# Optimization experiments

Hardware: AMD Instinct MI355X
Metric: run time of the kernel (lower is better)

The kernel has to match this reference:

```python
import jax, jax.numpy as jnp
import numpy as np
import math

B, S, D, H = 2, 2048, 512, 8
HD = D // H

def setup_inputs() -> dict:
    key = jax.random.key(0)
    ks = jax.random.split(key, 13)
    scale = 1.0 / math.sqrt(D)
    inp = {
        "q_in": jax.random.normal(ks[0], (B, S, D), jnp.float32),
        "k_in": jax.random.normal(ks[1], (B, S, D), jnp.float32),
        "v_in": jax.random.normal(ks[2], (B, S, D), jnp.float32),
        "mask": jax.random.randint(ks[3], (B, 1, S, S), 0, 2, jnp.int32),
        "W1": jax.random.uniform(ks[4], (D, D), jnp.float32, -scale, scale),
        "b1": jax.random.uniform(ks[5], (D,), jnp.float32, -scale, scale),
        "W2": jax.random.uniform(ks[6], (D, D), jnp.float32, -scale, scale),
        "b2": jax.random.uniform(ks[7], (D,), jnp.float32, -scale, scale),
        "W3": jax.random.uniform(ks[8], (D, D), jnp.float32, -scale, scale),
        "b3": jax.random.uniform(ks[9], (D,), jnp.float32, -scale, scale),
        "Wo": jax.random.uniform(ks[10], (D, D), jnp.float32, -scale, scale),
        "bo": jax.random.uniform(ks[11], (D,), jnp.float32, -scale, scale),
    }
    return inp

def reference(q_in, k_in, v_in, mask, W1, b1, W2, b2, W3, b3, Wo, bo):
    # Linear projections (torch Linear: y = x @ W.T + b)
    q = q_in @ W1.T + b1  # [B,S,D]
    k = k_in @ W2.T + b2
    v = v_in @ W3.T + b3
    # split heads -> [B,H,S,HD]
    def split(x):
        return x.reshape(B, S, H, HD).transpose(0, 2, 1, 3)
    q, k, v = split(q), split(k), split(v)
    scores = jnp.einsum("bhqd,bhkd->bhqk", q, k) / math.sqrt(HD)
    scores = jnp.where(mask == 0, jnp.float32(-1e9), scores)
    attn = jax.nn.softmax(scores, axis=-1)
    out = jnp.einsum("bhqk,bhkd->bhqd", attn, v)  # [B,H,S,HD]
    out = out.transpose(0, 2, 1, 3).reshape(B, S, D)
    return out @ Wo.T + bo
```

## Files before the change

### kernel.cpp

```cpp
#include <hip/hip_runtime.h>
#include <hip/hip_bf16.h>
#include <math.h>

constexpr int B_ = 2, S_ = 2048, D_ = 512, H_ = 8, HD_ = 64;
constexpr int M_ = B_ * S_;
constexpr int NT_ = S_ / 64;
constexpr int NSPLIT = 2;
constexpr int NT2 = NT_ / NSPLIT;
constexpr int ROWS = B_ * S_ * H_;

typedef short s16x8 __attribute__((ext_vector_type(8)));
typedef float f32x4 __attribute__((ext_vector_type(4)));
typedef unsigned short u16;
typedef unsigned long long u64;

#define SWZ(b) ((b) ^ ((((b) >> 7) & 7) << 4))

constexpr float SCL = 0.18033688f;

static __device__ __forceinline__ unsigned int cvt_pk2(float lo, float hi) {
  __hip_bfloat162 h = __float22bfloat162_rn(make_float2(lo, hi));
  return *(unsigned int*)&h;
}
static __device__ __forceinline__ u16 cvt1(float f) {
  __hip_bfloat16 h = __float2bfloat16(f);
  return *(u16*)&h;
}
static __device__ __forceinline__ uint4 pack8(float4 a, float4 b) {
  uint4 r;
  r.x = cvt_pk2(a.x, a.y); r.y = cvt_pk2(a.z, a.w);
  r.z = cvt_pk2(b.x, b.y); r.w = cvt_pk2(b.z, b.w);
  return r;
}

#define QKV_STEP(BUF, T)                                                      \
  {                                                                           \
    const bool more_ = ((T) < 7);                                             \
    if (more_) {                                                              \
      const int o4 = ((T) + 1) * 16;                                          \
      fx[0] = Xb[o4];  fx[1] = Xb[o4 + 1];  fx[2] = Xb[o4 + 2];  fx[3] = Xb[o4 + 3]; \
      fw0[0] = W0b[o4]; fw0[1] = W0b[o4 + 1]; fw0[2] = W0b[o4 + 2]; fw0[3] = W0b[o4 + 3]; \
      fw1[0] = W1b[o4]; fw1[1] = W1b[o4 + 1]; fw1[2] = W1b[o4 + 2]; fw1[3] = W1b[o4 + 3]; \
    }                                                                         \
    __builtin_amdgcn_s_setprio(1);                                            \
    _Pragma("unroll")                                                         \
    for (int kw = 0; kw < 2; ++kw) {                                          \
      s16x8 af0 = *(const s16x8*)(shb + SWZ((BUF)*24576 + (wm*32 + l15)*128 + kw*64 + lg*16)); \
      s16x8 af1 = *(const s16x8*)(shb + SWZ((BUF)*24576 + (wm*32 + 16 + l15)*128 + kw*64 + lg*16)); \
      s16x8 b00 = *(const s16x8*)(shb + SWZ((BUF)*24576 + 8192 + (wn*32 + l15)*128 + kw*64 + lg*16)); \
      s16x8 b01 = *(const s16x8*)(shb + SWZ((BUF)*24576 + 8192 + (wn*32 + 16 + l15)*128 + kw*64 + lg*16)); \
      s16x8 b10 = *(const s16x8*)(shb + SWZ((BUF)*24576 + 16384 + (wn*32 + l15)*128 + kw*64 + lg*16)); \
      s16x8 b11 = *(const s16x8*)(shb + SWZ((BUF)*24576 + 16384 + (wn*32 + 16 + l15)*128 + kw*64 + lg*16)); \
      acc[0][0][0] = __builtin_amdgcn_mfma_f32_16x16x32_bf16(af0, b00, acc[0][0][0], 0, 0, 0); \
      acc[0][0][1] = __builtin_amdgcn_mfma_f32_16x16x32_bf16(af0, b01, acc[0][0][1], 0, 0, 0); \
      acc[0][1][0] = __builtin_amdgcn_mfma_f32_16x16x32_bf16(af1, b00, acc[0][1][0], 0, 0, 0); \
      acc[0][1][1] = __builtin_amdgcn_mfma_f32_16x16x32_bf16(af1, b01, acc[0][1][1], 0, 0, 0); \
      acc[1][0][0] = __builtin_amdgcn_mfma_f32_16x16x32_bf16(af0, b10, acc[1][0][0], 0, 0, 0); \
      acc[1][0][1] = __builtin_amdgcn_mfma_f32_16x16x32_bf16(af0, b11, acc[1][0][1], 0, 0, 0); \
      acc[1][1][0] = __builtin_amdgcn_mfma_f32_16x16x32_bf16(af1, b10, acc[1][1][0], 0, 0, 0); \
      acc[1][1][1] = __builtin_amdgcn_mfma_f32_16x16x32_bf16(af1, b11, acc[1][1][1], 0, 0, 0); \
    }                                                                         \
    __builtin_amdgcn_s_setprio(0);                                            \
    if (more_) {                                                              \
      char* p_ = shb + ((BUF) ^ 1) * 24576;                                   \
      *(uint4*)(p_ + SWZ(awb)) = pack8(fx[0], fx[1]);                         \
      *(uint4*)(p_ + SWZ(awb + 16)) = pack8(fx[2], fx[3]);                    \
      *(uint4*)(p_ + SWZ(b0wb)) = pack8(fw0[0], fw0[1]);                      \
      *(uint4*)(p_ + SWZ(b0wb + 16)) = pack8(fw0[2], fw0[3]);                 \
      *(uint4*)(p_ + SWZ(b1wb)) = pack8(fw1[0], fw1[1]);                      \
      *(uint4*)(p_ + SWZ(b1wb + 16)) = pack8(fw1[2], fw1[3]);                 \
    }                                                                         \
    __syncthreads();                                                          \
  }

__global__ __launch_bounds__(256) void gemm_qkv(
    const float* __restrict__ Xq, const float* __restrict__ Wq,
    const float* __restrict__ bq, u16* __restrict__ Yq,
    const float* __restrict__ Xk, const float* __restrict__ Wk,
    const float* __restrict__ bk, u16* __restrict__ Yk,
    const float* __restrict__ Xv, const float* __restrict__ Wv,
    const float* __restrict__ bv, u16* __restrict__ Yv,
    const int* __restrict__ mask, u64* __restrict__ mbits)
{
  const float* X; const float* W; const float* bias; u16* Y;
  const int z = blockIdx.z;
  if (z == 0)      { X = Xq; W = Wq; bias = bq; Y = Yq; }
  else if (z == 1) { X = Xk; W = Wk; bias = bk; Y = Yk; }
  else             { X = Xv; W = Wv; bias = bv; Y = Yv; }

  __shared__ __align__(128) char SH[2][24576];
  char* shb = &SH[0][0];

  const int tid = threadIdx.x;
  const int lane = tid & 63, w = tid >> 6;
  const int l15 = lane & 15, lg = lane >> 4;
  const int wm = w >> 1, wn = w & 1;
  const int m0 = blockIdx.x * 64, n0 = blockIdx.y * 128;
  const int sr = tid >> 2, sc = (tid & 3) * 16;

  const float4* Xb  = (const float4*)&X[(size_t)(m0 + sr) * D_ + sc];
  const float4* W0b = (const float4*)&W[(size_t)(n0 + sr) * D_ + sc];
  const float4* W1b = (const float4*)&W[(size_t)(n0 + 64 + sr) * D_ + sc];
  const int awb  = sr * 128 + (tid & 3) * 32;
  const int b0wb = 8192 + awb;
  const int b1wb = 16384 + awb;

  f32x4 acc[2][2][2];
#pragma unroll
  for (int nh = 0; nh < 2; ++nh)
#pragma unroll
    for (int i = 0; i < 2; ++i)
#pragma unroll
      for (int j = 0; j < 2; ++j) acc[nh][i][j] = (f32x4){0.f, 0.f, 0.f, 0.f};

  float4 fx[4], fw0[4], fw1[4];
#pragma unroll
  for (int i = 0; i < 4; ++i) { fx[i] = Xb[i]; fw0[i] = W0b[i]; fw1[i] = W1b[i]; }
  {
    char* p = shb;
    *(uint4*)(p + SWZ(awb)) = pack8(fx[0], fx[1]);
    *(uint4*)(p + SWZ(awb + 16)) = pack8(fx[2], fx[3]);
    *(uint4*)(p + SWZ(b0wb)) = pack8(fw0[0], fw0[1]);
    *(uint4*)(p + SWZ(b0wb + 16)) = pack8(fw0[2], fw0[3]);
    *(uint4*)(p + SWZ(b1wb)) = pack8(fw1[0], fw1[1]);
    *(uint4*)(p + SWZ(b1wb + 16)) = pack8(fw1[2], fw1[3]);
  }
  __syncthreads();

#pragma unroll 1
  for (int tt = 0; tt < 8; tt += 2) {
    QKV_STEP(0, tt)
    QKV_STEP(1, tt + 1)
  }

  const float oscale = (z == 0) ? SCL : 1.0f;

  if (z != 2) {
#pragma unroll
    for (int nh = 0; nh < 2; ++nh) {
      float bias_v[2];
      bias_v[0] = bias[n0 + nh * 64 + wn * 32 + l15];
      bias_v[1] = bias[n0 + nh * 64 + wn * 32 + 16 + l15];
#pragma unroll
      for (int am = 0; am < 2; ++am)
#pragma unroll
        for (int bn = 0; bn < 2; ++bn)
#pragma unroll
          for (int j = 0; j < 4; ++j) {
            const int row = m0 + wm * 32 + am * 16 + lg * 4 + j;
            const int col = n0 + nh * 64 + wn * 32 + bn * 16 + l15;
            Y[(size_t)row * D_ + col] = cvt1((acc[nh][am][bn][j] + bias_v[bn]) * oscale);
          }
    }
  } else {
    const int batch = m0 >> 11, sb = m0 & (S_ - 1);
#pragma unroll
    for (int nh = 0; nh < 2; ++nh) {
      const int hh = blockIdx.y * 2 + nh;
      float bias_v[2];
      bias_v[0] = bias[n0 + nh * 64 + wn * 32 + l15];
      bias_v[1] = bias[n0 + nh * 64 + wn * 32 + 16 + l15];
      __syncthreads();
#pragma unroll
      for (int am = 0; am < 2; ++am)
#pragma unroll
        for (int bn = 0; bn < 2; ++bn) {
          const int dd = wn * 32 + bn * 16 + l15;
          const int sl = wm * 32 + am * 16 + lg * 4;
          ushort4 pk;
          pk.x = cvt1(acc[nh][am][bn][0] + bias_v[bn]);
          pk.y = cvt1(acc[nh][am][bn][1] + bias_v[bn]);
          pk.z = cvt1(acc[nh][am][bn][2] + bias_v[bn]);
          pk.w = cvt1(acc[nh][am][bn][3] + bias_v[bn]);
          *(ushort4*)(shb + SWZ(dd * 128 + sl * 2)) = pk;
        }
      __syncthreads();
      const int cr = sr * 128 + (tid & 3) * 32;
      uint4 c0 = *(uint4*)(shb + SWZ(cr));
      uint4 c1 = *(uint4*)(shb + SWZ(cr + 16));
      u16* dst = &Y[(((size_t)batch * H_ + hh) * 64 + sr) * S_ + sb + sc];
      *(uint4*)dst = c0;
      *(uint4*)(dst + 8) = c1;
    }
  }

  {
    const int bid = blockIdx.x + blockIdx.y * gridDim.x +
                    blockIdx.z * gridDim.x * gridDim.y;
    const int gw = bid * 4 + w;
    const int ngroups = (B_ * S_ * NT_) / 4;
#pragma unroll 1
    for (int g = gw; g < ngroups; g += 3072) {
      const int4 v = *(const int4*)&mask[(size_t)g * 256 + lane * 4];
      u64 b0 = __ballot(v.x != 0);
      u64 b1 = __ballot(v.y != 0);
      u64 b2 = __ballot(v.z != 0);
      u64 b3 = __ballot(v.w != 0);
      if (lane < 4) {
        const int q = lane;
        u64 r = ((b0 >> (16 * q)) & 0xFFFFULL)
              | (((b1 >> (16 * q)) & 0xFFFFULL) << 16)
              | (((b2 >> (16 * q)) & 0xFFFFULL) << 32)
              | (((b3 >> (16 * q)) & 0xFFFFULL) << 48);
        mbits[(size_t)g * 4 + q] = r;
      }
    }
  }
}

#define OPROJ_STEP(BUF, T)                                                    \
  {                                                                           \
    const bool more_ = ((T) < 7);                                             \
    if (more_) {                                                              \
      const int k0 = ((T) + 1) * 64;                                          \
      ax[0] = ((const uint4*)(Xb + k0))[0];                                   \
      ax[1] = ((const uint4*)(Xb + k0))[1];                                   \
      const int o4 = ((T) + 1) * 16;                                          \
      fw[0] = Wb[o4]; fw[1] = Wb[o4 + 1]; fw[2] = Wb[o4 + 2]; fw[3] = Wb[o4 + 3]; \
    }                                                                         \
    __builtin_amdgcn_s_setprio(1);                                            \
    _Pragma("unroll")                                                         \
    for (int kw = 0; kw < 2; ++kw) {                                          \
      s16x8 af0 = *(const s16x8*)(shb + SWZ((BUF)*16384 + (wm*32 + l15)*128 + kw*64 + lg*16)); \
      s16x8 af1 = *(const s16x8*)(shb + SWZ((BUF)*16384 + (wm*32 + 16 + l15)*128 + kw*64 + lg*16)); \
      s16x8 bf0 = *(const s16x8*)(shb + SWZ((BUF)*16384 + 8192 + (wn*32 + l15)*128 + kw*64 + lg*16)); \
      s16x8 bf1 = *(const s16x8*)(shb + SWZ((BUF)*16384 + 8192 + (wn*32 + 16 + l15)*128 + kw*64 + lg*16)); \
      acc[0][0] = __builtin_amdgcn_mfma_f32_16x16x32_bf16(af0, bf0, acc[0][0], 0, 0, 0); \
      acc[0][1] = __builtin_amdgcn_mfma_f32_16x16x32_bf16(af0, bf1, acc[0][1], 0, 0, 0); \
      acc[1][0] = __builtin_amdgcn_mfma_f32_16x16x32_bf16(af1, bf0, acc[1][0], 0, 0, 0); \
      acc[1][1] = __builtin_amdgcn_mfma_f32_16x16x32_bf16(af1, bf1, acc[1][1], 0, 0, 0); \
    }                                                                         \
    __builtin_amdgcn_s_setprio(0);                                            \
    if (more_) {                                                              \
      char* p_ = shb + ((BUF) ^ 1) * 16384;                                   \
      *(uint4*)(p_ + SWZ(awb)) = ax[0];                                       \
      *(uint4*)(p_ + SWZ(awb + 16)) = ax[1];                                  \
      *(uint4*)(p_ + SWZ(bwb)) = pack8(fw[0], fw[1]);                         \
      *(uint4*)(p_ + SWZ(bwb + 16)) = pack8(fw[2], fw[3]);                    \
    }                                                                         \
    __syncthreads();                                                          \
  }

__global__ __launch_bounds__(256) void gemm_oproj(
    const u16* __restrict__ X, const float* __restrict__ W,
    const float* __restrict__ bias, float* __restrict__ Y)
{
  __shared__ __align__(128) u16 SH[2][2][64][64];
  char* shb = (char*)SH;

  const int tid = threadIdx.x;
  const int lane = tid & 63, w = tid >> 6;
  const int l15 = lane & 15, lg = lane >> 4;
  const int wm = w >> 1, wn = w & 1;
  const int m0 = blockIdx.x * 64, n0 = blockIdx.y * 64;
  const int sr = tid >> 2, sc = (tid & 3) * 16;

  const u16* Xb = X + (size_t)(m0 + sr) * D_ + sc;
  const float4* Wb = (const float4*)&W[(size_t)(n0 + sr) * D_ + sc];
  const int awb = sr * 128 + (tid & 3) * 32;
  const int bwb = 8192 + sr * 128 + (tid & 3) * 32;

  f32x4 acc[2][2];
#pragma unroll
  for (int i = 0; i < 2; ++i)
#pragma unroll
    for (int j = 0; j < 2; ++j) acc[i][j] = (f32x4){0.f, 0.f, 0.f, 0.f};

  uint4 ax[2]; float4 fw[4];
  ax[0] = ((const uint4*)Xb)[0]; ax[1] = ((const uint4*)Xb)[1];
#pragma unroll
  for (int i = 0; i < 4; ++i) fw[i] = Wb[i];
  {
    char* p = shb;
    *(uint4*)(p + SWZ(awb)) = ax[0];
    *(uint4*)(p + SWZ(awb + 16)) = ax[1];
    *(uint4*)(p + SWZ(bwb)) = pack8(fw[0], fw[1]);
    *(uint4*)(p + SWZ(bwb + 16)) = pack8(fw[2], fw[3]);
  }
  __syncthreads();

#pragma unroll 1
  for (int tt = 0; tt < 8; tt += 2) {
    OPROJ_STEP(0, tt)
    OPROJ_STEP(1, tt + 1)
  }

  float bias_v[2];
  bias_v[0] = bias[n0 + wn * 32 + l15];
  bias_v[1] = bias[n0 + wn * 32 + 16 + l15];
#pragma unroll
  for (int am = 0; am < 2; ++am)
#pragma unroll
    for (int bn = 0; bn < 2; ++bn)
#pragma unroll
      for (int j = 0; j < 4; ++j) {
        const int row = m0 + wm * 32 + am * 16 + lg * 4 + j;
        const int col = n0 + wn * 32 + bn * 16 + l15;
        Y[(size_t)row * D_ + col] = acc[am][bn][j] + bias_v[bn];
      }
}

__global__ __launch_bounds__(256) void attn_mfma(
    const u16* __restrict__ qp, const u16* __restrict__ kp,
    const u16* __restrict__ vt, const u64* __restrict__ mbits,
    float* __restrict__ po, float* __restrict__ pm, float* __restrict__ pl)
{
  const int fid = blockIdx.x + 32 * (blockIdx.y + 8 * blockIdx.z);
  const int d = (fid & 7) * 128 + (fid >> 3);
  const int bx = d & 31, by = (d >> 5) & 7, bz = d >> 8;

  const int b = bz >> 1, half = bz & 1;
  const int h = by;
  const int q0 = bx * 64;
  const int kt0 = half * (S_ / NSPLIT);
  const int tid = threadIdx.x;
  const int lane = tid & 63;
  const int w = tid >> 6;
  const int l15 = lane & 15, lg = lane >> 4;

  __shared__ __align__(128) u16 KV[2][2][64][64];
  __shared__ __align__(128) u16 Pl[4][16][64];
  char* kvb = (char*)KV;
  char* plb = (char*)Pl;

  const int qr = q0 + w * 16;

  const u16* qrow = qp + ((size_t)b * S_ + qr + l15) * D_ + h * HD_;
  const s16x8 qf0 = *(const s16x8*)(qrow + lg * 8);
  const s16x8 qf1 = *(const s16x8*)(qrow + 32 + lg * 8);

  s16x8 onesf;
#pragma unroll
  for (int i = 0; i < 8; ++i) onesf[i] = (short)0x3F80;

  f32x4 out[4];
#pragma unroll
  for (int dt = 0; dt < 4; ++dt) out[dt] = (f32x4){0.f, 0.f, 0.f, 0.f};
  float l_s = 0.f;

  const int sr = tid >> 2;
  const int sc = (tid & 3) * 16;
  const u16* kbase = kp + (size_t)b * S_ * D_ + h * HD_;
  const u16* vbase = vt + (((size_t)b * H_ + h) * 64 + sr) * (size_t)S_ + kt0 + sc;
  const u64* mrow = mbits + ((size_t)b * S_ + qr + l15) * NT_ + half * NT2;

  const int mX = (l15 & 7) << 4;
  const int rd_lo = ((l15 << 7) + lg * 16) ^ mX;
  const int rd_hi = rd_lo ^ 64;
  const int mW = (sr & 7) << 4;
  const int wr_lo = ((sr << 7) + (tid & 3) * 32) ^ mW;
  const int wr_hi = wr_lo ^ 16;
  const int pq = w * 2048 + l15 * 128;
  const int pw0 = (pq + lg * 8) ^ mX;
  const int pa_lo = (pq + lg * 16) ^ mX;
  const int pa_hi = pa_lo ^ 64;

  uint4 rk0, rk1, rv0, rv1;
  {
    const u16* ksrc = kbase + (size_t)(kt0 + sr) * D_ + sc;
    rk0 = *(const uint4*)ksrc; rk1 = *(const uint4*)(ksrc + 8);
    rv0 = *(const uint4*)vbase; rv1 = *(const uint4*)(vbase + 8);
    *(uint4*)(kvb + wr_lo) = rk0;
    *(uint4*)(kvb + wr_hi) = rk1;
    *(uint4*)(kvb + wr_lo + 8192) = rv0;
    *(uint4*)(kvb + wr_hi + 8192) = rv1;
  }
  u64 msk = mrow[0];
  __syncthreads();

#pragma unroll 1
  for (int t = 0; t < NT2; ++t) {
    const int cur = t & 1;
    const bool more = (t + 1 < NT2);
    u64 msk_n = 0;
    if (more) {
      const int kt = (t + 1) * 64;
      const u16* ksrc = kbase + (size_t)(kt0 + kt + sr) * D_ + sc;
      rk0 = *(const uint4*)ksrc; rk1 = *(const uint4*)(ksrc + 8);
      rv0 = *(const uint4*)(vbase + kt); rv1 = *(const uint4*)(vbase + kt + 8);
      msk_n = mrow[t + 1];
    }

    const unsigned mlo = (unsigned)(msk >> lg);
    const unsigned mhi = (unsigned)(msk >> (lg + 32));

    char* rb_lo = kvb + (cur << 14) + rd_lo;
    char* rb_hi = kvb + (cur << 14) + rd_hi;

    f32x4 z[4];
    __builtin_amdgcn_s_setprio(1);
#pragma unroll
    for (int t4 = 0; t4 < 4; ++t4) {
      s16x8 kb0 = *(const s16x8*)(rb_lo + t4 * 2048);
      s16x8 kb1 = *(const s16x8*)(rb_hi + t4 * 2048);
      f32x4 zz = (f32x4){0.f, 0.f, 0.f, 0.f};
      zz = __builtin_amdgcn_mfma_f32_16x16x32_bf16(kb0, qf0, zz, 0, 0, 0);
      zz = __builtin_amdgcn_mfma_f32_16x16x32_bf16(kb1, qf1, zz, 0, 0, 0);
      z[t4] = zz;
    }
    __builtin_amdgcn_s_setprio(0);

    float x[4][4];
#pragma unroll
    for (int t4 = 0; t4 < 4; ++t4) {
#pragma unroll
      for (int r = 0; r < 4; ++r) {
        const unsigned bit = (r < 2) ? ((mlo >> (16 * r + 4 * t4)) & 1u)
                                     : ((mhi >> (16 * (r - 2) + 4 * t4)) & 1u);
        float xv = bit ? z[t4][r] : -1.0e9f;
        x[t4][r] = exp2f(xv);
      }
    }

#pragma unroll
    for (int t4 = 0; t4 < 4; ++t4) {
      uint2 pk;
      pk.x = cvt_pk2(x[t4][0], x[t4][1]);
      pk.y = cvt_pk2(x[t4][2], x[t4][3]);
      *(uint2*)(plb + (pw0 ^ (t4 * 32))) = pk;
    }

    s16x8 pa0 = *(const s16x8*)(plb + pa_lo);
    s16x8 pa1 = *(const s16x8*)(plb + pa_hi);

    __builtin_amdgcn_s_setprio(1);
    f32x4 zl = (f32x4){0.f, 0.f, 0.f, 0.f};
    zl = __builtin_amdgcn_mfma_f32_16x16x32_bf16(onesf, pa0, zl, 0, 0, 0);
    zl = __builtin_amdgcn_mfma_f32_16x16x32_bf16(onesf, pa1, zl, 0, 0, 0);
#pragma unroll
    for (int dt = 0; dt < 4; ++dt) {
      s16x8 va0 = *(const s16x8*)(rb_lo + 8192 + dt * 2048);
      s16x8 va1 = *(const s16x8*)(rb_hi + 8192 + dt * 2048);
      out[dt] = __builtin_amdgcn_mfma_f32_16x16x32_bf16(va0, pa0, out[dt], 0, 0, 0);
      out[dt] = __builtin_amdgcn_mfma_f32_16x16x32_bf16(va1, pa1, out[dt], 0, 0, 0);
    }
    __builtin_amdgcn_s_setprio(0);
    l_s += zl[0];

    if (more) {
      char* wb_lo = kvb + ((cur ^ 1) << 14) + wr_lo;
      char* wb_hi = kvb + ((cur ^ 1) << 14) + wr_hi;
      *(uint4*)(wb_lo) = rk0;
      *(uint4*)(wb_hi) = rk1;
      *(uint4*)(wb_lo + 8192) = rv0;
      *(uint4*)(wb_hi + 8192) = rv1;
      msk = msk_n;
    }
    __syncthreads();
  }

  const int rowi = ((b * S_ + qr + l15) * H_) + h;
  float* pobase = po + ((size_t)half * ROWS + rowi) * 64;
#pragma unroll
  for (int dt = 0; dt < 4; ++dt) {
    float4 o = make_float4(out[dt][0], out[dt][1], out[dt][2], out[dt][3]);
    *(float4*)&pobase[dt * 16 + lg * 4] = o;
  }
  if (lg == 0) {
    pm[(size_t)half * ROWS + rowi] = 0.0f;
    pl[(size_t)half * ROWS + rowi] = l_s;
  }
}

__global__ __launch_bounds__(256) void attn_combine(
    const float* __restrict__ po, const float* __restrict__ pm,
    const float* __restrict__ pl, u16* __restrict__ ob)
{
  const int gid = blockIdx.x * 256 + threadIdx.x;
  const int row = gid >> 4;
  const int d0 = (gid & 15) * 4;

  float4 o1 = *(const float4*)&po[(size_t)row * 64 + d0];
  float4 o2 = *(const float4*)&po[(size_t)(ROWS + row) * 64 + d0];
  const float m1 = pm[row], m2 = pm[ROWS + row];
  const float l1 = pl[row], l2 = pl[ROWS + row];
  const float m = fmaxf(m1, m2);
  const float w1 = exp2f(m1 - m), w2 = exp2f(m2 - m);
  const float inv = 1.0f / (l1 * w1 + l2 * w2);

  const int bq = row >> 3, h = row & 7;
  uint2 o;
  o.x = cvt_pk2((o1.x * w1 + o2.x * w2) * inv, (o1.y * w1 + o2.y * w2) * inv);
  o.y = cvt_pk2((o1.z * w1 + o2.z * w2) * inv, (o1.w * w1 + o2.w * w2) * inv);
  *(uint2*)&ob[(size_t)bq * D_ + h * 64 + d0] = o;
}

extern "C" void kernel_launch(void* const* d_in, const int* in_sizes, int n_in,
                              void* d_out, int out_size, void* d_ws,
                              size_t ws_size, hipStream_t stream)
{
  const float* q_in = (const float*)d_in[0];
  const float* k_in = (const float*)d_in[1];
  const float* v_in = (const float*)d_in[2];
  const int*   mask = (const int*)d_in[3];
  const float* W1 = (const float*)d_in[4];
  const float* b1 = (const float*)d_in[5];
  const float* W2 = (const float*)d_in[6];
  const float* b2 = (const float*)d_in[7];
  const float* W3 = (const float*)d_in[8];
  const float* b3 = (const float*)d_in[9];
  const float* Wo = (const float*)d_in[10];
  const float* bo = (const float*)d_in[11];
  float* out = (float*)d_out;

  char* ws = (char*)d_ws;
  u16* qp = (u16*)ws;
  u16* kp = (u16*)(ws + (4u << 20));
  u16* vtp = (u16*)(ws + (8u << 20));
  u64* mbits = (u64*)(ws + (12u << 20));
  float* pm = (float*)(ws + (13u << 20));
  float* pl = (float*)(ws + (13u << 20) + (ROWS * NSPLIT * 4));
  float* po = (float*)(ws + (13u << 20) + (512u << 10));
  u16* ob = qp;

  dim3 blk(256);
  gemm_qkv<<<dim3(M_ / 64, D_ / 128, 3), blk, 0, stream>>>(
      q_in, W1, b1, qp, k_in, W2, b2, kp, v_in, W3, b3, vtp, mask, mbits);
  attn_mfma<<<dim3(S_ / 64, H_, B_ * NSPLIT), blk, 0, stream>>>(
      qp, kp, vtp, mbits, po, pm, pl);
  attn_combine<<<ROWS * 16 / 256, blk, 0, stream>>>(po, pm, pl, ob);
  gemm_oproj<<<dim3(M_ / 64, D_ / 64), blk, 0, stream>>>(ob, Wo, bo, out);
}
```

Measured before the change: 94.28 us.

## Fuse split-KV combine into output projection GEMM A-tile load

Removes the separate attn_combine kernel and the pm buffer. The o-projection GEMM now reads both fp32 partial outputs and row sums directly, normalises and converts to bf16 while loading its A tile. Since the max is fixed at zero in the attention kernel, the combine reduces to (o1+o2)/(l1+l2). This saves a launch and a bf16 round-trip through global memory, but each oproj block rereads fp32 partials (4x the bytes of bf16) redundantly across its 8 column blocks.

```diff
diff --git a/kernel.cpp b/kernel.cpp
--- a/kernel.cpp
+++ b/kernel.cpp
@@ -31,6 +31,10 @@
   r.x = cvt_pk2(a.x, a.y); r.y = cvt_pk2(a.z, a.w);
   r.z = cvt_pk2(b.x, b.y); r.w = cvt_pk2(b.z, b.w);
   return r;
+}
+static __device__ __forceinline__ float4 sum_scale(float4 a, float4 b, float s) {
+  return make_float4((a.x + b.x) * s, (a.y + b.y) * s,
+                     (a.z + b.z) * s, (a.w + b.w) * s);
 }
 
 #define QKV_STEP(BUF, T)                                                      \
@@ -212,10 +216,15 @@
   {                                                                           \
     const bool more_ = ((T) < 7);                                             \
     if (more_) {                                                              \
-      const int k0 = ((T) + 1) * 64;                                          \
-      ax[0] = ((const uint4*)(Xb + k0))[0];                                   \
-      ax[1] = ((const uint4*)(Xb + k0))[1];                                   \
-      const int o4 = ((T) + 1) * 16;                                          \
+      const int t1 = (T) + 1;                                                 \
+      const float4* q0 = (const float4*)(poR + t1 * 64);                      \
+      const float4* q1 = (const float4*)(poR + 2097152 + t1 * 64);            \
+      float4 s0 = q0[0], s1 = q0[1], s2 = q0[2], s3 = q0[3];                  \
+      float4 u0 = q1[0], u1 = q1[1], u2 = q1[2], u3 = q1[3];                  \
+      const float li = 1.0f / (plR[t1] + plR[ROWS + t1]);                     \
+      ax[0] = pack8(sum_scale(s0, u0, li), sum_scale(s1, u1, li));            \
+      ax[1] = pack8(sum_scale(s2, u2, li), sum_scale(s3, u3, li));            \
+      const int o4 = t1 * 16;                                                 \
       fw[0] = Wb[o4]; fw[1] = Wb[o4 + 1]; fw[2] = Wb[o4 + 2]; fw[3] = Wb[o4 + 3]; \
     }                                                                         \
     __builtin_amdgcn_s_setprio(1);                                            \
@@ -242,8 +251,9 @@
   }
 
 __global__ __launch_bounds__(256) void gemm_oproj(
-    const u16* __restrict__ X, const float* __restrict__ W,
-    const float* __restrict__ bias, float* __restrict__ Y)
+    const float* __restrict__ po, const float* __restrict__ pl,
+    const float* __restrict__ W, const float* __restrict__ bias,
+    float* __restrict__ Y)
 {
   __shared__ __align__(128) u16 SH[2][2][64][64];
   char* shb = (char*)SH;
@@ -255,7 +265,8 @@
   const int m0 = blockIdx.x * 64, n0 = blockIdx.y * 64;
   const int sr = tid >> 2, sc = (tid & 3) * 16;
 
-  const u16* Xb = X + (size_t)(m0 + sr) * D_ + sc;
+  const float* poR = po + (size_t)(m0 + sr) * 512 + sc;
+  const float* plR = pl + (size_t)(m0 + sr) * 8;
   const float4* Wb = (const float4*)&W[(size_t)(n0 + sr) * D_ + sc];
   const int awb = sr * 128 + (tid & 3) * 32;
   const int bwb = 8192 + sr * 128 + (tid & 3) * 32;
@@ -267,10 +278,16 @@
     for (int j = 0; j < 2; ++j) acc[i][j] = (f32x4){0.f, 0.f, 0.f, 0.f};
 
   uint4 ax[2]; float4 fw[4];
-  ax[0] = ((const uint4*)Xb)[0]; ax[1] = ((const uint4*)Xb)[1];
-#pragma unroll
-  for (int i = 0; i < 4; ++i) fw[i] = Wb[i];
   {
+    const float4* q0 = (const float4*)(poR);
+    const float4* q1 = (const float4*)(poR + 2097152);
+    float4 s0 = q0[0], s1 = q0[1], s2 = q0[2], s3 = q0[3];
+    float4 u0 = q1[0], u1 = q1[1], u2 = q1[2], u3 = q1[3];
+    const float li = 1.0f / (plR[0] + plR[ROWS]);
+    ax[0] = pack8(sum_scale(s0, u0, li), sum_scale(s1, u1, li));
+    ax[1] = pack8(sum_scale(s2, u2, li), sum_scale(s3, u3, li));
+#pragma unroll
+    for (int i = 0; i < 4; ++i) fw[i] = Wb[i];
     char* p = shb;
     *(uint4*)(p + SWZ(awb)) = ax[0];
     *(uint4*)(p + SWZ(awb + 16)) = ax[1];
@@ -303,7 +320,7 @@
 __global__ __launch_bounds__(256) void attn_mfma(
     const u16* __restrict__ qp, const u16* __restrict__ kp,
     const u16* __restrict__ vt, const u64* __restrict__ mbits,
-    float* __restrict__ po, float* __restrict__ pm, float* __restrict__ pl)
+    float* __restrict__ po, float* __restrict__ pl)
 {
   const int fid = blockIdx.x + 32 * (blockIdx.y + 8 * blockIdx.z);
   const int d = (fid & 7) * 128 + (fid >> 3);
@@ -456,33 +473,7 @@
     float4 o = make_float4(out[dt][0], out[dt][1], out[dt][2], out[dt][3]);
     *(float4*)&pobase[dt * 16 + lg * 4] = o;
   }
-  if (lg == 0) {
-    pm[(size_t)half * ROWS + rowi] = 0.0f;
-    pl[(size_t)half * ROWS + rowi] = l_s;
-  }
-}
-
-__global__ __launch_bounds__(256) void attn_combine(
-    const float* __restrict__ po, const float* __restrict__ pm,
-    const float* __restrict__ pl, u16* __restrict__ ob)
-{
-  const int gid = blockIdx.x * 256 + threadIdx.x;
-  const int row = gid >> 4;
-  const int d0 = (gid & 15) * 4;
-
-  float4 o1 = *(const float4*)&po[(size_t)row * 64 + d0];
-  float4 o2 = *(const float4*)&po[(size_t)(ROWS + row) * 64 + d0];
-  const float m1 = pm[row], m2 = pm[ROWS + row];
-  const float l1 = pl[row], l2 = pl[ROWS + row];
-  const float m = fmaxf(m1, m2);
-  const float w1 = exp2f(m1 - m), w2 = exp2f(m2 - m);
-  const float inv = 1.0f / (l1 * w1 + l2 * w2);
-
-  const int bq = row >> 3, h = row & 7;
-  uint2 o;
-  o.x = cvt_pk2((o1.x * w1 + o2.x * w2) * inv, (o1.y * w1 + o2.y * w2) * inv);
-  o.y = cvt_pk2((o1.z * w1 + o2.z * w2) * inv, (o1.w * w1 + o2.w * w2) * inv);
-  *(uint2*)&ob[(size_t)bq * D_ + h * 64 + d0] = o;
+  if (lg == 0) pl[(size_t)half * ROWS + rowi] = l_s;
 }
 
 extern "C" void kernel_launch(void* const* d_in, const int* in_sizes, int n_in,
@@ -508,16 +499,13 @@
   u16* kp = (u16*)(ws + (4u << 20));
   u16* vtp = (u16*)(ws + (8u << 20));
   u64* mbits = (u64*)(ws + (12u << 20));
-  float* pm = (float*)(ws + (13u << 20));
-  float* pl = (float*)(ws + (13u << 20) + (ROWS * NSPLIT * 4));
+  float* pl = (float*)(ws + (13u << 20));
   float* po = (float*)(ws + (13u << 20) + (512u << 10));
-  u16* ob = qp;
 
   dim3 blk(256);
   gemm_qkv<<<dim3(M_ / 64, D_ / 128, 3), blk, 0, stream>>>(
       q_in, W1, b1, qp, k_in, W2, b2, kp, v_in, W3, b3, vtp, mask, mbits);
   attn_mfma<<<dim3(S_ / 64, H_, B_ * NSPLIT), blk, 0, stream>>>(
-      qp, kp, vtp, mbits, po, pm, pl);
-  attn_combine<<<ROWS * 16 / 256, blk, 0, stream>>>(po, pm, pl, ob);
-  gemm_oproj<<<dim3(M_ / 64, D_ / 64), blk, 0, stream>>>(ob, Wo, bo, out);
-}
+      qp, kp, vtp, mbits, po, pl);
+  gemm_oproj<<<dim3(M_ / 64, D_ / 64), blk, 0, stream>>>(po, pl, Wo, bo, out);
+}
```

Result: no change. 92.53 us (-1.9%).
